# Performance work log

Hardware: AMD Instinct MI355X
Metric: run time of the kernel (lower is better)

## Reference

```python
import jax, jax.numpy as jnp
import numpy as np
import math
from itertools import combinations_with_replacement

# ---- module constants (init: d_key=16, d_val=64, p=2, is_causal=True) ----
D_KEY, D_VAL, P = 16, 64, 2
B, H, N = 1, 8, 4096

# M: multisets of size p over d_key indices -> [m, p], m = comb(d_key+p-1, p) = 136
M_NP = np.array(list(combinations_with_replacement(range(D_KEY), P)), dtype=np.int64)

def _n_multiset_perms(row):
    counts = np.bincount(row, minlength=D_KEY)
    denom = 1
    for c in counts:
        denom *= math.factorial(int(c))
    return math.factorial(P) / denom

C_NP = np.array([_n_multiset_perms(r) for r in M_NP], dtype=np.float32)  # [m]
ALPHA = np.float32(1.0 / (math.factorial(P) * D_KEY ** (P / 2)))
M_J = jnp.asarray(M_NP)
C_J = jnp.asarray(C_NP)


def _phi(x):
    # x: [..., d_key] -> polynomial features [..., m] via gather + product over p indices
    return jnp.prod(x[..., M_J], axis=-1)


def setup_inputs() -> dict:
    key = jax.random.key(0)
    kq, kk, kv = jax.random.split(key, 3)
    Q = jax.random.normal(kq, (B, H, N, D_KEY), dtype=jnp.float32)
    K = jax.random.normal(kk, (B, H, N, D_KEY), dtype=jnp.float32)
    V = jax.random.normal(kv, (B, H, N, D_VAL), dtype=jnp.float32)
    return {"Q": Q, "K": K, "V": V, "continue_prev": 0}


def reference(Q, K, V, continue_prev):
    # continue_prev is False (0): fresh sequence, no carried state.
    Phi_Q = _phi(Q)  # [b,h,n,m]
    Phi_K = _phi(K)  # [b,h,n,m]
    # causal accumulation: cumsum over token axis (-3)
    H_S = jnp.cumsum(Phi_K[..., None] * V[..., None, :], axis=-3) * ALPHA  # [b,h,n,m,d_val]
    H_Z = jnp.cumsum(Phi_K[..., None], axis=-3) * ALPHA                    # [b,h,n,m,1]
    S_term = jnp.einsum('m,bhnm,bhnmd->bhnd', C_J, Phi_Q, H_S)  # [b,h,n,d_val]
    Z_term = jnp.einsum('m,bhnm,bhnmd->bhnd', C_J, Phi_Q, H_Z)  # [b,h,n,1]
    return (S_term, Z_term)
```

## Files before the change

kernel.cpp:

```cpp
#include <hip/hip_runtime.h>


#define SEQN 4096
#define NHEAD 8
#define DKEY 16
#define DVAL 64
#define CHUNK 128
#define NCHUNK 32
#define ALPHA 0.03125f

typedef float f32x4 __attribute__((ext_vector_type(4)));
typedef __bf16 bf16x4 __attribute__((ext_vector_type(4)));
typedef __bf16 bf16x8 __attribute__((ext_vector_type(8)));
typedef unsigned long long u64;
typedef u64 u64x2 __attribute__((ext_vector_type(2)));

#define SW512(row, colb) (((row) << 9) + ((colb) ^ (((row) & 7) << 4)))
#define SW256(row, colb) (((row) << 8) + ((colb) ^ (((row) & 7) << 4)))

__device__ inline float bf2f(__bf16 x) {
    unsigned short u = __builtin_bit_cast(unsigned short, x);
    unsigned int v = ((unsigned int)u) << 16;
    return __builtin_bit_cast(float, v);
}

__global__ __launch_bounds__(512, 1)
void p01_state(const float* __restrict__ Kg, const float* __restrict__ Vg,
               __bf16* __restrict__ Kbf, __bf16* __restrict__ Vtg,
               __bf16* __restrict__ G)
{
    __shared__ __align__(128) unsigned char Vt2[80 * 256];
    __shared__ __align__(128) unsigned char Ktf[16 * 512];
    const int tid = threadIdx.x;
    const int w = tid >> 6;
    const int lane = tid & 63;
    const int r = lane & 15, g = lane >> 4;
    const int bid = blockIdx.x;
    const int h = bid & 7, c = bid >> 3;
    const int k0 = c * CHUNK;

    {
        const int key = tid >> 2, part = tid & 3;
        const float* kp = Kg + ((size_t)h * SEQN + k0 + key) * DKEY + 4 * part;
        const f32x4 a = *(const f32x4*)kp;
        #pragma unroll
        for (int j = 0; j < 4; ++j)
            *(float*)(Ktf + SW512(4 * part + j, key * 4)) = a[j];
        bf16x4 o;
        #pragma unroll
        for (int j = 0; j < 4; ++j) o[j] = (__bf16)a[j];
        *(bf16x4*)&Kbf[((size_t)h * SEQN + k0 + key) * DKEY + 4 * part] = o;
    }
    {
        const int el = tid & 63;
        const int seg = tid >> 6;
        const float* __restrict__ Vh = Vg + (size_t)h * SEQN * DVAL;
        #pragma unroll
        for (int p = 0; p < 2; ++p) {
            const int tb = 8 * (seg + 8 * p);
            bf16x8 v;
            #pragma unroll
            for (int j = 0; j < 8; ++j)
                v[j] = (__bf16)Vh[(size_t)(k0 + tb + j) * DVAL + el];
            *(bf16x8*)(Vt2 + SW256(el, tb * 2)) = v;
        }
    }
    {
        const int row = 64 + (tid >> 5);
        const int i = tid & 31;
        const u64 val = (row == 64) ? 0x3F803F803F803F80ULL : 0ULL;
        *(u64*)(Vt2 + SW256(row, 8 * i)) = val;
    }
    __syncthreads();

    #pragma unroll
    for (int uu = 0; uu < 2; ++uu) {
        const int unit = 2 * tid + uu;
        const int m = unit & 3;
        const int hsel = (unit >> 2) & 1;
        const int ktl = (unit >> 3) & 1;
        const int dloc = unit >> 4;
        const u64 t0v = *(const u64*)(Vt2 + SW256(dloc, 128 * ktl + 64 * hsel + 8 * m));
        const u64 t1v = *(const u64*)(Vt2 + SW256(dloc, 128 * ktl + 64 * hsel + 8 * m + 32));
        __bf16* vo = Vtg + ((size_t)((h * 64 + 2 * c + ktl) * 64 + dloc)) * 64 + hsel * 32;
        u64x2 pp; pp[0] = t0v; pp[1] = t1v;
        *(u64x2*)((u64*)vo + 2 * m) = pp;
    }

    f32x4 acc[2][5] = {};
    #pragma unroll
    for (int ks = 0; ks < 4; ++ks) {
        const int t0 = 32 * ks + 8 * g;
        bf16x8 af[5];
        #pragma unroll
        for (int et = 0; et < 5; ++et)
            af[et] = *(const bf16x8*)(Vt2 + SW256(16 * et + r, t0 * 2));
        const f32x4 kra = *(const f32x4*)(Ktf + SW512(r, t0 * 4));
        const f32x4 krb = *(const f32x4*)(Ktf + SW512(r, t0 * 4 + 16));
        #pragma unroll
        for (int fa = 0; fa < 2; ++fa) {
            const int ft = 2 * w + fa;
            const f32x4 kfa = *(const f32x4*)(Ktf + SW512(ft, t0 * 4));
            const f32x4 kfb = *(const f32x4*)(Ktf + SW512(ft, t0 * 4 + 16));
            bf16x8 bfrag;
            #pragma unroll
            for (int j = 0; j < 4; ++j) {
                bfrag[j]     = (__bf16)(kfa[j] * kra[j]);
                bfrag[4 + j] = (__bf16)(kfb[j] * krb[j]);
            }
            #pragma unroll
            for (int et = 0; et < 5; ++et)
                acc[fa][et] = __builtin_amdgcn_mfma_f32_16x16x32_bf16(
                    bfrag, af[et], acc[fa][et], 0, 0, 0);
        }
    }
    __bf16* Gc = G + (size_t)(h * NCHUNK + c) * 20480;
    #pragma unroll
    for (int fa = 0; fa < 2; ++fa) {
        const int wfa = 2 * w + fa;
        #pragma unroll
        for (int et = 0; et < 5; ++et) {
            bf16x4 o;
            #pragma unroll
            for (int i = 0; i < 4; ++i) o[i] = (__bf16)acc[fa][et][i];
            *(bf16x4*)&Gc[((wfa * 5 + et) * 64 + lane) * 4] = o;
        }
    }
}

__global__ __launch_bounds__(256)
void p2_scan(const __bf16* __restrict__ G, __bf16* __restrict__ Hb)
{
    const int h = blockIdx.x & 7;
    const int fb = blockIdx.x >> 3;
    const int fid = fb * 1024 + 4 * threadIdx.x;
    const __bf16* Gh = G + (size_t)h * NCHUNK * 20480 + fid;
    __bf16* Hh = Hb + (size_t)h * NCHUNK * 20480 + fid;
    f32x4 acc = {};
    #pragma unroll
    for (int cc = 0; cc < NCHUNK; ++cc) {
        bf16x4 o;
        #pragma unroll
        for (int j = 0; j < 4; ++j) o[j] = (__bf16)acc[j];
        *(bf16x4*)&Hh[cc * 20480] = o;
        const bf16x4 v = *(const bf16x4*)&Gh[cc * 20480];
        #pragma unroll
        for (int j = 0; j < 4; ++j) acc[j] += bf2f(v[j]);
    }
}


#define LOADKV(KT, KF, VF)                                                        \
    {                                                                             \
        const __bf16* Kb_ = Kbf + ((size_t)h * SEQN + (KT) * 64) * DKEY;          \
        const __bf16* Vb_ = Vtg + (size_t)((h * 64 + (KT)) * 64) * 64;            \
        _Pragma("unroll")                                                         \
        for (int ks_ = 0; ks_ < 2; ++ks_) {                                       \
            _Pragma("unroll")                                                     \
            for (int uk_ = 0; uk_ < 2; ++uk_) {                                   \
                bf16x8 f_ = {};                                                   \
                if (g < 2)                                                        \
                    f_ = *(const bf16x8*)&Kb_[(32 * ks_ + 16 * uk_ + r) * DKEY + 8 * g]; \
                KF[ks_][uk_] = f_;                                                \
            }                                                                     \
            _Pragma("unroll")                                                     \
            for (int dt_ = 0; dt_ < 4; ++dt_)                                     \
                VF[ks_][dt_] = *(const bf16x8*)&Vb_[(size_t)(16 * dt_ + r) * 64 + 32 * ks_ + 8 * g]; \
        }                                                                         \
    }

__global__ __launch_bounds__(256, 2)
void p3m_attend(const float* __restrict__ Qg, const __bf16* __restrict__ Kbf,
                const __bf16* __restrict__ Vtg, const __bf16* __restrict__ Hb,
                float* __restrict__ Og)
{
    __shared__ __align__(128) unsigned char Hlds[80 * 512];
    const int tid = threadIdx.x;
    const int lane = tid & 63;
    const int r = lane & 15, g = lane >> 4;
    const int w = tid >> 6;
    const int bid = blockIdx.x;
    const int h = bid & 7;
    const int x = bid >> 3;
    const int c = x >> 1;
    const int qh = x & 1;
    const int qb = c * CHUNK + qh * 64 + 16 * w;

    float qr[16];
    {
        const float* qp = Qg + ((size_t)h * SEQN + qb + r) * DKEY;
        #pragma unroll
        for (int m = 0; m < 4; ++m) {
            const f32x4 v = *(const f32x4*)(qp + 4 * m);
            qr[4 * m + 0] = v[0]; qr[4 * m + 1] = v[1];
            qr[4 * m + 2] = v[2]; qr[4 * m + 3] = v[3];
        }
    }
    float qsel[8];
    #pragma unroll
    for (int j = 0; j < 8; ++j) qsel[j] = (g & 1) ? qr[8 + j] : qr[j];
    bf16x8 qfrag = {};
    if (g < 2) {
        #pragma unroll
        for (int j = 0; j < 8; ++j) qfrag[j] = (__bf16)qsel[j];
    }

    bf16x8 kf0[2][2], vf0[2][4], kf1[2][2], vf1[2][4];
    LOADKV(2 * c, kf0, vf0);

    if (c > 0) {
        const __bf16* Hbc = Hb + (size_t)(h * NCHUNK + c) * 20480;
        #pragma unroll
        for (int k2 = 0; k2 < 10; ++k2) {
            const int U = tid + 256 * k2;
            const int wfa = U / 160;
            const int rem = U - wfa * 160;
            const int et = rem >> 5;
            const int lp = rem & 31;
            const int L0 = 2 * lp, L1 = L0 + 1;
            const int e0 = 16 * et + (L0 & 15), f0 = 16 * wfa + 4 * (L0 >> 4);
            const int e1 = 16 * et + (L1 & 15), f1 = 16 * wfa + 4 * (L1 >> 4);
            const u64x2 v = *(const u64x2*)&Hbc[U * 8];
            *(u64*)(Hlds + SW512(e0, 2 * f0)) = v[0];
            *(u64*)(Hlds + SW512(e1, 2 * f1)) = v[1];
        }
    }
    if (qh == 1) LOADKV(2 * c + 1, kf1, vf1);

    f32x4 oacc[4] = {};
    f32x4 zacc4 = {};
    float zin = 0.f;

    if (c > 0) {
        __syncthreads();
        #pragma unroll
        for (int ks = 0; ks < 8; ++ks) {
            const int t0 = 32 * ks + 8 * g;
            bf16x8 af[4];
            #pragma unroll
            for (int dt = 0; dt < 4; ++dt)
                af[dt] = *(const bf16x8*)(Hlds + SW512(16 * dt + r, t0 * 2));
            const bf16x8 afz = *(const bf16x8*)(Hlds + SW512(64 + r, t0 * 2));
            const float qi = ALPHA * ((g & 2) ? qr[2 * ks + 1] : qr[2 * ks]);
            bf16x8 pf;
            #pragma unroll
            for (int j = 0; j < 8; ++j) pf[j] = (__bf16)(qi * qsel[j]);
            #pragma unroll
            for (int dt = 0; dt < 4; ++dt)
                oacc[dt] = __builtin_amdgcn_mfma_f32_16x16x32_bf16(af[dt], pf, oacc[dt], 0, 0, 0);
            zacc4 = __builtin_amdgcn_mfma_f32_16x16x32_bf16(afz, pf, zacc4, 0, 0, 0);
        }
    }

    const int qG = qb + r;
    const int qlocmax = qh * 64 + 16 * w + 15;
    #pragma unroll
    for (int tl = 0; tl < 2; ++tl) {
        if (tl <= qh) {
            const bool diag = (tl == qh);
            const int k0g = (2 * c + tl) * 64;
            #pragma unroll
            for (int ks = 0; ks < 2; ++ks) {
                if (64 * tl + 32 * ks <= qlocmax) {
                    const f32x4 zero4 = {};
                    f32x4 s[2];
                    #pragma unroll
                    for (int uk = 0; uk < 2; ++uk)
                        s[uk] = __builtin_amdgcn_mfma_f32_16x16x32_bf16(
                            (tl == 0) ? kf0[ks][uk] : kf1[ks][uk], qfrag, zero4, 0, 0, 0);
                    bf16x8 pf;
                    float zs = 0.f;
                    #pragma unroll
                    for (int uk = 0; uk < 2; ++uk) {
                        const int kGb = k0g + 32 * ks + 16 * uk + 4 * g;
                        #pragma unroll
                        for (int i = 0; i < 4; ++i) {
                            const float sv = s[uk][i];
                            float p = ALPHA * sv * sv;
                            if (diag && (kGb + i > qG)) p = 0.f;
                            zs += p;
                            pf[4 * uk + i] = (__bf16)p;
                        }
                    }
                    zin += zs;
                    #pragma unroll
                    for (int dt = 0; dt < 4; ++dt)
                        oacc[dt] = __builtin_amdgcn_mfma_f32_16x16x32_bf16(
                            (tl == 0) ? vf0[ks][dt] : vf1[ks][dt], pf, oacc[dt], 0, 0, 0);
                }
            }
        }
    }

    const int q = qb + r;
    #pragma unroll
    for (int dt = 0; dt < 4; ++dt) {
        float* op = Og + ((size_t)h * SEQN + q) * DVAL + 16 * dt + 4 * g;
        *(f32x4*)op = oacc[dt];
    }
    zin += __shfl_xor(zin, 16); zin += __shfl_xor(zin, 32);
    if (lane < 16) {
        float* zp = Og + (size_t)NHEAD * SEQN * DVAL + (size_t)h * SEQN + qb;
        zp[r] = zin + zacc4[0];
    }
}

__global__ __launch_bounds__(128, 2)
void taylor_mono(const float* __restrict__ Qg, const float* __restrict__ Kg,
                 const float* __restrict__ Vg, float* __restrict__ Og)
{
    __shared__ __align__(16) __bf16 Kl[64 * 32];
    __shared__ __align__(16) __bf16 Vt[64 * 72];
    typedef __bf16 bf16x2 __attribute__((ext_vector_type(2)));
    const int tid = threadIdx.x;
    const int wv = tid >> 6;
    const int lane = tid & 63;
    const int r = lane & 15, g = lane >> 4;
    const int bid = blockIdx.x;
    const int h = bid & 7;
    const int tt = bid >> 3;
    const int qt = (tt & 1) ? (tt >> 1) : (63 - (tt >> 1));
    const int qb = qt * 64 + wv * 32;
    const float* __restrict__ Qh = Qg + (size_t)h * SEQN * DKEY;
    const float* __restrict__ Kh = Kg + (size_t)h * SEQN * DKEY;
    const float* __restrict__ Vh = Vg + (size_t)h * SEQN * DVAL;
    for (int row = tid; row < 64; row += 128) {
        bf16x8 z = {};
        *(bf16x8*)&Kl[row * 32 + 16] = z;
        *(bf16x8*)&Kl[row * 32 + 24] = z;
    }
    bf16x8 qfrag[2];
    #pragma unroll
    for (int uq = 0; uq < 2; ++uq) {
        bf16x8 f = {};
        if (g < 2) {
            const float* qp = Qh + (size_t)(qb + 16 * uq + r) * DKEY + 8 * g;
            const f32x4 a = *(const f32x4*)qp;
            const f32x4 b = *(const f32x4*)(qp + 4);
            #pragma unroll
            for (int j = 0; j < 4; ++j) { f[j] = (__bf16)a[j]; f[4 + j] = (__bf16)b[j]; }
        }
        qfrag[uq] = f;
    }
    f32x4 oacc[2][4] = {};
    float zacc0 = 0.f, zacc1 = 0.f;
    const int nkt = qt + 1;
    for (int kt = 0; kt < nkt; ++kt) {
        const int k0 = kt * 64;
        {
            const int key = tid >> 1, half = tid & 1;
            const float* kp = Kh + (size_t)(k0 + key) * DKEY + 8 * half;
            const f32x4 a = *(const f32x4*)kp;
            const f32x4 b = *(const f32x4*)(kp + 4);
            bf16x8 kb;
            #pragma unroll
            for (int j = 0; j < 4; ++j) { kb[j] = (__bf16)a[j]; kb[4 + j] = (__bf16)b[j]; }
            *(bf16x8*)&Kl[key * 32 + 8 * half] = kb;
        }
        {
            const int d = tid & 63;
            const int kp2 = (tid >> 6) * 2;
            #pragma unroll
            for (int i = 0; i < 16; ++i) {
                const int kk = i * 4 + kp2;
                const float a0 = Vh[(size_t)(k0 + kk) * DVAL + d];
                const float a1 = Vh[(size_t)(k0 + kk + 1) * DVAL + d];
                const int w32 = kk & 31;
                const int col = (kk & 32) + ((w32 >> 2) & 3) * 8 + ((w32 >> 4) << 2) + (kk & 3);
                bf16x2 p; p[0] = (__bf16)a0; p[1] = (__bf16)a1;
                *(bf16x2*)&Vt[d * 72 + col] = p;
            }
        }
        __syncthreads();
        const bool diag = (kt + 1 == nkt);
        #pragma unroll
        for (int ks = 0; ks < 2; ++ks) {
            if (k0 + 32 * ks < qb + 32) {
                bf16x8 vfrag[4];
                #pragma unroll
                for (int dt = 0; dt < 4; ++dt)
                    vfrag[dt] = *(const bf16x8*)&Vt[(16 * dt + r) * 72 + 32 * ks + 8 * g];
                bf16x8 kfr[2];
                #pragma unroll
                for (int uk = 0; uk < 2; ++uk)
                    kfr[uk] = *(const bf16x8*)&Kl[(32 * ks + 16 * uk + r) * 32 + 8 * g];
                const f32x4 zero4 = {};
                f32x4 s[2][2];
                #pragma unroll
                for (int uq = 0; uq < 2; ++uq)
                    #pragma unroll
                    for (int uk = 0; uk < 2; ++uk)
                        s[uq][uk] = __builtin_amdgcn_mfma_f32_16x16x32_bf16(
                            kfr[uk], qfrag[uq], zero4, 0, 0, 0);
                #pragma unroll
                for (int uq = 0; uq < 2; ++uq) {
                    bf16x8 pf;
                    float zs = 0.f;
                    #pragma unroll
                    for (int uk = 0; uk < 2; ++uk) {
                        const int kGb = k0 + 32 * ks + 16 * uk + 4 * g;
                        const int qG = qb + 16 * uq + r;
                        #pragma unroll
                        for (int i = 0; i < 4; ++i) {
                            const float sv = s[uq][uk][i];
                            float p = 0.03125f * sv * sv;
                            if (diag && (kGb + i > qG)) p = 0.f;
                            zs += p;
                            pf[4 * uk + i] = (__bf16)p;
                        }
                    }
                    if (uq == 0) zacc0 += zs; else zacc1 += zs;
                    #pragma unroll
                    for (int dt = 0; dt < 4; ++dt)
                        oacc[uq][dt] = __builtin_amdgcn_mfma_f32_16x16x32_bf16(
                            vfrag[dt], pf, oacc[uq][dt], 0, 0, 0);
                }
            }
        }
        __syncthreads();
    }
    #pragma unroll
    for (int uq = 0; uq < 2; ++uq) {
        const int q = qb + 16 * uq + r;
        #pragma unroll
        for (int dt = 0; dt < 4; ++dt) {
            float* op = Og + ((size_t)h * SEQN + q) * DVAL + 16 * dt + 4 * g;
            *(f32x4*)op = oacc[uq][dt];
        }
    }
    zacc0 += __shfl_xor(zacc0, 16); zacc0 += __shfl_xor(zacc0, 32);
    zacc1 += __shfl_xor(zacc1, 16); zacc1 += __shfl_xor(zacc1, 32);
    if (lane < 16) {
        float* zp = Og + (size_t)NHEAD * SEQN * DVAL + (size_t)h * SEQN + qb;
        zp[r] = zacc0;
        zp[16 + r] = zacc1;
    }
}

extern "C" void kernel_launch(void* const* d_in, const int* in_sizes, int n_in,
                              void* d_out, int out_size, void* d_ws, size_t ws_size,
                              hipStream_t stream) {
    const float* Q = (const float*)d_in[0];
    const float* K = (const float*)d_in[1];
    const float* V = (const float*)d_in[2];
    float* O = (float*)d_out;

    const size_t G_OFF   = 0;
    const size_t HB_OFF  = 10485760;
    const size_t KBF_OFF = 20971520;
    const size_t VTG_OFF = 22020096;
    const size_t NEED    = 26214400;

    if (ws_size >= NEED) {
        char* ws = (char*)d_ws;
        __bf16* G   = (__bf16*)(ws + G_OFF);
        __bf16* Hb  = (__bf16*)(ws + HB_OFF);
        __bf16* Kbf = (__bf16*)(ws + KBF_OFF);
        __bf16* Vtg = (__bf16*)(ws + VTG_OFF);
        p01_state <<<dim3(256), dim3(512), 0, stream>>>(K, V, Kbf, Vtg, G);
        p2_scan   <<<dim3(160), dim3(256), 0, stream>>>(G, Hb);
        p3m_attend<<<dim3(512), dim3(256), 0, stream>>>(Q, Kbf, Vtg, Hb, O);
    } else {
        taylor_mono<<<dim3(512), dim3(128), 0, stream>>>(Q, K, V, O);
    }
}
```

Baseline: 30.90 us.

## Fuse intra-chunk causal attention into the state kernel and drop K/V staging buffers

Measured after the change: 28.40 us. 1.09x faster.

```diff
diff --git a/kernel.cpp b/kernel.cpp
--- a/kernel.cpp
+++ b/kernel.cpp
@@ -26,11 +26,12 @@
 
 __global__ __launch_bounds__(512, 1)
 void p01_state(const float* __restrict__ Kg, const float* __restrict__ Vg,
-               __bf16* __restrict__ Kbf, __bf16* __restrict__ Vtg,
-               __bf16* __restrict__ G)
+               const float* __restrict__ Qg, __bf16* __restrict__ G,
+               float* __restrict__ Og)
 {
     __shared__ __align__(128) unsigned char Vt2[80 * 256];
     __shared__ __align__(128) unsigned char Ktf[16 * 512];
+    __shared__ __align__(128) unsigned char Kl[128 * 32];
     const int tid = threadIdx.x;
     const int w = tid >> 6;
     const int lane = tid & 63;
@@ -38,6 +39,18 @@
     const int bid = blockIdx.x;
     const int h = bid & 7, c = bid >> 3;
     const int k0 = c * CHUNK;
+    const int qb = k0 + 16 * w;
+
+    float qr[16];
+    {
+        const float* qp = Qg + ((size_t)h * SEQN + qb + r) * DKEY;
+        #pragma unroll
+        for (int m = 0; m < 4; ++m) {
+            const f32x4 v = *(const f32x4*)(qp + 4 * m);
+            qr[4 * m + 0] = v[0]; qr[4 * m + 1] = v[1];
+            qr[4 * m + 2] = v[2]; qr[4 * m + 3] = v[3];
+        }
+    }
 
     {
         const int key = tid >> 2, part = tid & 3;
@@ -49,7 +62,7 @@
         bf16x4 o;
         #pragma unroll
         for (int j = 0; j < 4; ++j) o[j] = (__bf16)a[j];
-        *(bf16x4*)&Kbf[((size_t)h * SEQN + k0 + key) * DKEY + 4 * part] = o;
+        *(bf16x4*)(Kl + key * 32 + ((8 * part) ^ ((key & 1) << 4))) = o;
     }
     {
         const int el = tid & 63;
@@ -73,58 +86,123 @@
     }
     __syncthreads();
 
-    #pragma unroll
-    for (int uu = 0; uu < 2; ++uu) {
-        const int unit = 2 * tid + uu;
-        const int m = unit & 3;
-        const int hsel = (unit >> 2) & 1;
-        const int ktl = (unit >> 3) & 1;
-        const int dloc = unit >> 4;
-        const u64 t0v = *(const u64*)(Vt2 + SW256(dloc, 128 * ktl + 64 * hsel + 8 * m));
-        const u64 t1v = *(const u64*)(Vt2 + SW256(dloc, 128 * ktl + 64 * hsel + 8 * m + 32));
-        __bf16* vo = Vtg + ((size_t)((h * 64 + 2 * c + ktl) * 64 + dloc)) * 64 + hsel * 32;
-        u64x2 pp; pp[0] = t0v; pp[1] = t1v;
-        *(u64x2*)((u64*)vo + 2 * m) = pp;
-    }
-
-    f32x4 acc[2][5] = {};
-    #pragma unroll
-    for (int ks = 0; ks < 4; ++ks) {
-        const int t0 = 32 * ks + 8 * g;
-        bf16x8 af[5];
-        #pragma unroll
-        for (int et = 0; et < 5; ++et)
-            af[et] = *(const bf16x8*)(Vt2 + SW256(16 * et + r, t0 * 2));
-        const f32x4 kra = *(const f32x4*)(Ktf + SW512(r, t0 * 4));
-        const f32x4 krb = *(const f32x4*)(Ktf + SW512(r, t0 * 4 + 16));
+    {
+        f32x4 acc[2][5] = {};
+        #pragma unroll
+        for (int ks = 0; ks < 4; ++ks) {
+            const int t0 = 32 * ks + 8 * g;
+            bf16x8 af[5];
+            #pragma unroll
+            for (int et = 0; et < 5; ++et)
+                af[et] = *(const bf16x8*)(Vt2 + SW256(16 * et + r, t0 * 2));
+            const f32x4 kra = *(const f32x4*)(Ktf + SW512(r, t0 * 4));
+            const f32x4 krb = *(const f32x4*)(Ktf + SW512(r, t0 * 4 + 16));
+            #pragma unroll
+            for (int fa = 0; fa < 2; ++fa) {
+                const int ft = 2 * w + fa;
+                const f32x4 kfa = *(const f32x4*)(Ktf + SW512(ft, t0 * 4));
+                const f32x4 kfb = *(const f32x4*)(Ktf + SW512(ft, t0 * 4 + 16));
+                bf16x8 bfrag;
+                #pragma unroll
+                for (int j = 0; j < 4; ++j) {
+                    bfrag[j]     = (__bf16)(kfa[j] * kra[j]);
+                    bfrag[4 + j] = (__bf16)(kfb[j] * krb[j]);
+                }
+                #pragma unroll
+                for (int et = 0; et < 5; ++et)
+                    acc[fa][et] = __builtin_amdgcn_mfma_f32_16x16x32_bf16(
+                        bfrag, af[et], acc[fa][et], 0, 0, 0);
+            }
+        }
+        __bf16* Gc = G + (size_t)(h * NCHUNK + c) * 20480;
         #pragma unroll
         for (int fa = 0; fa < 2; ++fa) {
-            const int ft = 2 * w + fa;
-            const f32x4 kfa = *(const f32x4*)(Ktf + SW512(ft, t0 * 4));
-            const f32x4 kfb = *(const f32x4*)(Ktf + SW512(ft, t0 * 4 + 16));
-            bf16x8 bfrag;
-            #pragma unroll
-            for (int j = 0; j < 4; ++j) {
-                bfrag[j]     = (__bf16)(kfa[j] * kra[j]);
-                bfrag[4 + j] = (__bf16)(kfb[j] * krb[j]);
+            const int wfa = 2 * w + fa;
+            #pragma unroll
+            for (int et = 0; et < 5; ++et) {
+                bf16x4 o;
+                #pragma unroll
+                for (int i = 0; i < 4; ++i) o[i] = (__bf16)acc[fa][et][i];
+                *(bf16x4*)&Gc[((wfa * 5 + et) * 64 + lane) * 4] = o;
             }
-            #pragma unroll
-            for (int et = 0; et < 5; ++et)
-                acc[fa][et] = __builtin_amdgcn_mfma_f32_16x16x32_bf16(
-                    bfrag, af[et], acc[fa][et], 0, 0, 0);
-        }
-    }
-    __bf16* Gc = G + (size_t)(h * NCHUNK + c) * 20480;
-    #pragma unroll
-    for (int fa = 0; fa < 2; ++fa) {
-        const int wfa = 2 * w + fa;
-        #pragma unroll
-        for (int et = 0; et < 5; ++et) {
-            bf16x4 o;
-            #pragma unroll
-            for (int i = 0; i < 4; ++i) o[i] = (__bf16)acc[fa][et][i];
-            *(bf16x4*)&Gc[((wfa * 5 + et) * 64 + lane) * 4] = o;
-        }
+        }
+    }
+
+    float qsel[8];
+    #pragma unroll
+    for (int j = 0; j < 8; ++j) qsel[j] = (g & 1) ? qr[8 + j] : qr[j];
+    bf16x8 qfrag = {};
+    if (g < 2) {
+        #pragma unroll
+        for (int j = 0; j < 8; ++j) qfrag[j] = (__bf16)qsel[j];
+    }
+
+    f32x4 oacc[4] = {};
+    float zin = 0.f;
+    const int qG = qb + r;
+    const int smax = w >> 1;
+    #pragma unroll
+    for (int tl = 0; tl < 2; ++tl) {
+        #pragma unroll
+        for (int ks = 0; ks < 2; ++ks) {
+            const int sidx = 2 * tl + ks;
+            if (sidx <= smax) {
+                const bool diag = (sidx == smax);
+                bf16x8 kf[2];
+                #pragma unroll
+                for (int uk = 0; uk < 2; ++uk) {
+                    bf16x8 f = {};
+                    if (g < 2) {
+                        const int key = 64 * tl + 32 * ks + 16 * uk + r;
+                        f = *(const bf16x8*)(Kl + key * 32 + ((16 * g) ^ ((key & 1) << 4)));
+                    }
+                    kf[uk] = f;
+                }
+                const f32x4 zero4 = {};
+                f32x4 s[2];
+                #pragma unroll
+                for (int uk = 0; uk < 2; ++uk)
+                    s[uk] = __builtin_amdgcn_mfma_f32_16x16x32_bf16(kf[uk], qfrag, zero4, 0, 0, 0);
+
+                bf16x8 pf;
+                float zs = 0.f;
+                const int k0g = k0 + 64 * tl + 32 * ks;
+                #pragma unroll
+                for (int uk = 0; uk < 2; ++uk) {
+                    const int kGb = k0g + 16 * uk + 4 * g;
+                    #pragma unroll
+                    for (int i = 0; i < 4; ++i) {
+                        const float sv = s[uk][i];
+                        float p = ALPHA * sv * sv;
+                        if (diag && (kGb + i > qG)) p = 0.f;
+                        zs += p;
+                        pf[4 * uk + i] = (__bf16)p;
+                    }
+                }
+                zin += zs;
+                #pragma unroll
+                for (int dt = 0; dt < 4; ++dt) {
+                    const int base = 128 * tl + 64 * ks + 8 * g;
+                    u64x2 both;
+                    both[0] = *(const u64*)(Vt2 + SW256(16 * dt + r, base));
+                    both[1] = *(const u64*)(Vt2 + SW256(16 * dt + r, base + 32));
+                    const bf16x8 vf = __builtin_bit_cast(bf16x8, both);
+                    oacc[dt] = __builtin_amdgcn_mfma_f32_16x16x32_bf16(vf, pf, oacc[dt], 0, 0, 0);
+                }
+            }
+        }
+    }
+
+    const int q = qb + r;
+    #pragma unroll
+    for (int dt = 0; dt < 4; ++dt) {
+        float* op = Og + ((size_t)h * SEQN + q) * DVAL + 16 * dt + 4 * g;
+        *(f32x4*)op = oacc[dt];
+    }
+    zin += __shfl_xor(zin, 16); zin += __shfl_xor(zin, 32);
+    if (lane < 16) {
+        float* zp = Og + (size_t)NHEAD * SEQN * DVAL + (size_t)h * SEQN + qb;
+        zp[r] = zin;
     }
 }
 
@@ -149,30 +227,9 @@
     }
 }
 
-
-#define LOADKV(KT, KF, VF)                                                        \
-    {                                                                             \
-        const __bf16* Kb_ = Kbf + ((size_t)h * SEQN + (KT) * 64) * DKEY;          \
-        const __bf16* Vb_ = Vtg + (size_t)((h * 64 + (KT)) * 64) * 64;            \
-        _Pragma("unroll")                                                         \
-        for (int ks_ = 0; ks_ < 2; ++ks_) {                                       \
-            _Pragma("unroll")                                                     \
-            for (int uk_ = 0; uk_ < 2; ++uk_) {                                   \
-                bf16x8 f_ = {};                                                   \
-                if (g < 2)                                                        \
-                    f_ = *(const bf16x8*)&Kb_[(32 * ks_ + 16 * uk_ + r) * DKEY + 8 * g]; \
-                KF[ks_][uk_] = f_;                                                \
-            }                                                                     \
-            _Pragma("unroll")                                                     \
-            for (int dt_ = 0; dt_ < 4; ++dt_)                                     \
-                VF[ks_][dt_] = *(const bf16x8*)&Vb_[(size_t)(16 * dt_ + r) * 64 + 32 * ks_ + 8 * g]; \
-        }                                                                         \
-    }
-
 __global__ __launch_bounds__(256, 2)
-void p3m_attend(const float* __restrict__ Qg, const __bf16* __restrict__ Kbf,
-                const __bf16* __restrict__ Vtg, const __bf16* __restrict__ Hb,
-                float* __restrict__ Og)
+void p3s_apply(const float* __restrict__ Qg, const __bf16* __restrict__ Hb,
+               float* __restrict__ Og)
 {
     __shared__ __align__(128) unsigned char Hlds[80 * 512];
     const int tid = threadIdx.x;
@@ -184,11 +241,13 @@
     const int x = bid >> 3;
     const int c = x >> 1;
     const int qh = x & 1;
+    if (c == 0) return;
     const int qb = c * CHUNK + qh * 64 + 16 * w;
+    const int q = qb + r;
 
     float qr[16];
     {
-        const float* qp = Qg + ((size_t)h * SEQN + qb + r) * DKEY;
+        const float* qp = Qg + ((size_t)h * SEQN + q) * DKEY;
         #pragma unroll
         for (int m = 0; m < 4; ++m) {
             const f32x4 v = *(const f32x4*)(qp + 4 * m);
@@ -196,19 +255,14 @@
             qr[4 * m + 2] = v[2]; qr[4 * m + 3] = v[3];
         }
     }
-    float qsel[8];
-    #pragma unroll
-    for (int j = 0; j < 8; ++j) qsel[j] = (g & 1) ? qr[8 + j] : qr[j];
-    bf16x8 qfrag = {};
-    if (g < 2) {
-        #pragma unroll
-        for (int j = 0; j < 8; ++j) qfrag[j] = (__bf16)qsel[j];
-    }
-
-    bf16x8 kf0[2][2], vf0[2][4], kf1[2][2], vf1[2][4];
-    LOADKV(2 * c, kf0, vf0);
-
-    if (c > 0) {
+    f32x4 oprev[4];
+    #pragma unroll
+    for (int dt = 0; dt < 4; ++dt)
+        oprev[dt] = *(const f32x4*)(Og + ((size_t)h * SEQN + q) * DVAL + 16 * dt + 4 * g);
+    float* zp = Og + (size_t)NHEAD * SEQN * DVAL + (size_t)h * SEQN + qb;
+    const float zprev = zp[r];
+
+    {
         const __bf16* Hbc = Hb + (size_t)(h * NCHUNK + c) * 20480;
         #pragma unroll
         for (int k2 = 0; k2 < 10; ++k2) {
@@ -225,84 +279,41 @@
             *(u64*)(Hlds + SW512(e1, 2 * f1)) = v[1];
         }
     }
-    if (qh == 1) LOADKV(2 * c + 1, kf1, vf1);
-
+    __syncthreads();
+
+    float qsel[8];
+    #pragma unroll
+    for (int j = 0; j < 8; ++j) qsel[j] = (g & 1) ? qr[8 + j] : qr[j];
     f32x4 oacc[4] = {};
     f32x4 zacc4 = {};
-    float zin = 0.f;
-
-    if (c > 0) {
-        __syncthreads();
-        #pragma unroll
-        for (int ks = 0; ks < 8; ++ks) {
-            const int t0 = 32 * ks + 8 * g;
-            bf16x8 af[4];
-            #pragma unroll
-            for (int dt = 0; dt < 4; ++dt)
-                af[dt] = *(const bf16x8*)(Hlds + SW512(16 * dt + r, t0 * 2));
-            const bf16x8 afz = *(const bf16x8*)(Hlds + SW512(64 + r, t0 * 2));
-            const float qi = ALPHA * ((g & 2) ? qr[2 * ks + 1] : qr[2 * ks]);
-            bf16x8 pf;
-            #pragma unroll
-            for (int j = 0; j < 8; ++j) pf[j] = (__bf16)(qi * qsel[j]);
-            #pragma unroll
-            for (int dt = 0; dt < 4; ++dt)
-                oacc[dt] = __builtin_amdgcn_mfma_f32_16x16x32_bf16(af[dt], pf, oacc[dt], 0, 0, 0);
-            zacc4 = __builtin_amdgcn_mfma_f32_16x16x32_bf16(afz, pf, zacc4, 0, 0, 0);
-        }
-    }
-
-    const int qG = qb + r;
-    const int qlocmax = qh * 64 + 16 * w + 15;
-    #pragma unroll
-    for (int tl = 0; tl < 2; ++tl) {
-        if (tl <= qh) {
-            const bool diag = (tl == qh);
-            const int k0g = (2 * c + tl) * 64;
-            #pragma unroll
-            for (int ks = 0; ks < 2; ++ks) {
-                if (64 * tl + 32 * ks <= qlocmax) {
-                    const f32x4 zero4 = {};
-                    f32x4 s[2];
-                    #pragma unroll
-                    for (int uk = 0; uk < 2; ++uk)
-                        s[uk] = __builtin_amdgcn_mfma_f32_16x16x32_bf16(
-                            (tl == 0) ? kf0[ks][uk] : kf1[ks][uk], qfrag, zero4, 0, 0, 0);
-                    bf16x8 pf;
-                    float zs = 0.f;
-                    #pragma unroll
-                    for (int uk = 0; uk < 2; ++uk) {
-                        const int kGb = k0g + 32 * ks + 16 * uk + 4 * g;
-                        #pragma unroll
-                        for (int i = 0; i < 4; ++i) {
-                            const float sv = s[uk][i];
-                            float p = ALPHA * sv * sv;
-                            if (diag && (kGb + i > qG)) p = 0.f;
-                            zs += p;
-                            pf[4 * uk + i] = (__bf16)p;
-                        }
-                    }
-                    zin += zs;
-                    #pragma unroll
-                    for (int dt = 0; dt < 4; ++dt)
-                        oacc[dt] = __builtin_amdgcn_mfma_f32_16x16x32_bf16(
-                            (tl == 0) ? vf0[ks][dt] : vf1[ks][dt], pf, oacc[dt], 0, 0, 0);
-                }
-            }
-        }
-    }
-
-    const int q = qb + r;
+    #pragma unroll
+    for (int ks = 0; ks < 8; ++ks) {
+        const int t0 = 32 * ks + 8 * g;
+        bf16x8 af[4];
+        #pragma unroll
+        for (int dt = 0; dt < 4; ++dt)
+            af[dt] = *(const bf16x8*)(Hlds + SW512(16 * dt + r, t0 * 2));
+        const bf16x8 afz = *(const bf16x8*)(Hlds + SW512(64 + r, t0 * 2));
+        const float qi = ALPHA * ((g & 2) ? qr[2 * ks + 1] : qr[2 * ks]);
+        bf16x8 pf;
+        #pragma unroll
+        for (int j = 0; j < 8; ++j) pf[j] = (__bf16)(qi * qsel[j]);
+        #pragma unroll
+        for (int dt = 0; dt < 4; ++dt)
+            oacc[dt] = __builtin_amdgcn_mfma_f32_16x16x32_bf16(af[dt], pf, oacc[dt], 0, 0, 0);
+        zacc4 = __builtin_amdgcn_mfma_f32_16x16x32_bf16(afz, pf, zacc4, 0, 0, 0);
+    }
+
     #pragma unroll
     for (int dt = 0; dt < 4; ++dt) {
         float* op = Og + ((size_t)h * SEQN + q) * DVAL + 16 * dt + 4 * g;
-        *(f32x4*)op = oacc[dt];
-    }
-    zin += __shfl_xor(zin, 16); zin += __shfl_xor(zin, 32);
-    if (lane < 16) {
-        float* zp = Og + (size_t)NHEAD * SEQN * DVAL + (size_t)h * SEQN + qb;
-        zp[r] = zin + zacc4[0];
-    }
+        f32x4 o = oprev[dt];
+        #pragma unroll
+        for (int i = 0; i < 4; ++i) o[i] += oacc[dt][i];
+        *(f32x4*)op = o;
+    }
+    if (lane < 16)
+        zp[r] = zprev + zacc4[0];
 }
 
 __global__ __launch_bounds__(128, 2)
@@ -445,21 +456,17 @@
     const float* V = (const float*)d_in[2];
     float* O = (float*)d_out;
 
-    const size_t G_OFF   = 0;
-    const size_t HB_OFF  = 10485760;
-    const size_t KBF_OFF = 20971520;
-    const size_t VTG_OFF = 22020096;
-    const size_t NEED    = 26214400;
+    const size_t G_OFF  = 0;
+    const size_t HB_OFF = 10485760;
+    const size_t NEED   = 20971520;
 
     if (ws_size >= NEED) {
         char* ws = (char*)d_ws;
-        __bf16* G   = (__bf16*)(ws + G_OFF);
-        __bf16* Hb  = (__bf16*)(ws + HB_OFF);
-        __bf16* Kbf = (__bf16*)(ws + KBF_OFF);
-        __bf16* Vtg = (__bf16*)(ws + VTG_OFF);
-        p01_state <<<dim3(256), dim3(512), 0, stream>>>(K, V, Kbf, Vtg, G);
-        p2_scan   <<<dim3(160), dim3(256), 0, stream>>>(G, Hb);
-        p3m_attend<<<dim3(512), dim3(256), 0, stream>>>(Q, Kbf, Vtg, Hb, O);
+        __bf16* G  = (__bf16*)(ws + G_OFF);
+        __bf16* Hb = (__bf16*)(ws + HB_OFF);
+        p01_state<<<dim3(256), dim3(512), 0, stream>>>(K, V, Q, G, O);
+        p2_scan  <<<dim3(160), dim3(256), 0, stream>>>(G, Hb);
+        p3s_apply<<<dim3(512), dim3(256), 0, stream>>>(Q, Hb, O);
     } else {
         taylor_mono<<<dim3(512), dim3(128), 0, stream>>>(Q, K, V, O);
     }
```
